# Performance work log

Hardware: AMD Instinct MI355X
Metric: run time of the kernel (lower is better)

Reference implementation:

```python
import jax, jax.numpy as jnp
import numpy as np
from jax import lax

EPS = 1e-3  # Keras BatchNormalization default epsilon
DN = ('NHWC', 'HWIO', 'NHWC')


def _bn(x, gamma, beta, mean, var):
    inv = gamma * lax.rsqrt(var + EPS)
    return x * inv + (beta - mean * inv)


def setup_inputs() -> dict:
    key = jax.random.key(0)
    ks = jax.random.split(key, 5)
    B, H, W, C = 32, 56, 56, 256
    G, CG = 32, 4  # cardinality, channels per group
    CM = G * CG    # 128 mid channels
    x = jax.random.normal(ks[0], (B, H, W, C), jnp.float32)
    # 32 branch 1x1 convs (256->4 each) stacked -> one 256->128 conv
    w1 = jax.random.normal(ks[1], (1, 1, C, CM), jnp.float32) * 0.05
    b1 = jnp.zeros((CM,), jnp.float32)
    g1 = jnp.ones((CM,), jnp.float32)
    be1 = jnp.zeros((CM,), jnp.float32)
    m1 = jnp.zeros((CM,), jnp.float32)
    v1 = jnp.ones((CM,), jnp.float32)
    # 32 branch 3x3 convs (4->4 each) stacked -> grouped conv kernel [3,3,4,128]
    w2 = jax.random.normal(ks[2], (3, 3, CG, CM), jnp.float32) * 0.1
    b2 = jnp.zeros((CM,), jnp.float32)
    g2 = jnp.ones((CM,), jnp.float32)
    be2 = jnp.zeros((CM,), jnp.float32)
    m2 = jnp.zeros((CM,), jnp.float32)
    v2 = jnp.ones((CM,), jnp.float32)
    # final 1x1 conv 128 -> 256
    w3 = jax.random.normal(ks[3], (1, 1, CM, C), jnp.float32) * 0.05
    b3 = jnp.zeros((C,), jnp.float32)
    return dict(x=x, w1=w1, b1=b1, g1=g1, be1=be1, m1=m1, v1=v1,
                w2=w2, b2=b2, g2=g2, be2=be2, m2=m2, v2=v2,
                w3=w3, b3=b3)


def reference(x, w1, b1, g1, be1, m1, v1, w2, b2, g2, be2, m2, v2, w3, b3):
    # branch 1x1 convs fused: conv 256 -> 128
    h = lax.conv_general_dilated(x, w1, (1, 1), 'SAME', dimension_numbers=DN) + b1
    h = jax.nn.relu(_bn(h, g1, be1, m1, v1))
    # branch 3x3 convs fused: grouped conv, 32 groups of 4 channels
    h = lax.conv_general_dilated(h, w2, (1, 1), 'SAME', dimension_numbers=DN,
                                 feature_group_count=32) + b2
    h = jax.nn.relu(_bn(h, g2, be2, m2, v2))
    # Dropout(0.2) is identity at inference
    # final 1x1 conv 128 -> 256, residual add, relu
    out = lax.conv_general_dilated(h, w3, (1, 1), 'SAME', dimension_numbers=DN) + b3
    return jax.nn.relu(out + x)
```

## Files before the change

### kernel.cpp

```cpp
#include <hip/hip_runtime.h>
#include <stdint.h>

typedef unsigned short u16;
typedef unsigned int   u32;
typedef __attribute__((ext_vector_type(8))) short bf16x8;
typedef __attribute__((ext_vector_type(4))) float f32x4;

#define EPS 1e-3f
#define NB 32
#define HW 56
#define CI 256
#define CM 128
#define PIX (NB*HW*HW)

__device__ __forceinline__ float asf(u32 i){ union{u32 u; float f;} t; t.u=i; return t.f; }
__device__ __forceinline__ u16 f2bf(float f){
  union{float f; u32 u;} t; t.f = f;
  u32 x = t.u;
  return (u16)((x + 0x7fffu + ((x>>16)&1u)) >> 16);
}

__global__ __launch_bounds__(256) void kprep(
    const float* __restrict__ w1, const float* __restrict__ b1, const float* __restrict__ g1,
    const float* __restrict__ be1, const float* __restrict__ m1, const float* __restrict__ v1,
    const float* __restrict__ b2, const float* __restrict__ g2,
    const float* __restrict__ be2, const float* __restrict__ m2, const float* __restrict__ v2,
    const float* __restrict__ w3,
    u16* __restrict__ w1s, u16* __restrict__ w3s,
    float* __restrict__ A1, float* __restrict__ B1,
    float* __restrict__ A2, float* __restrict__ B2){
  int i = blockIdx.x*256 + threadIdx.x;
  if (i < 32768){
    {
      int j = i & 7, lane = (i >> 3) & 63, kt = (i >> 9) & 7, t = i >> 12;
      int col = lane & 15, quad = lane >> 4;
      int n = t*16 + col, k = kt*32 + quad*8 + j;
      w1s[i] = f2bf(w1[k*CM + n]);
    }
    {
      int j = i & 7, lane = (i >> 3) & 63, kc = (i >> 9) & 3, t = i >> 11;
      int col = lane & 15, quad = lane >> 4;
      int n = t*16 + col, k = kc*32 + quad*8 + j;
      w3s[i] = f2bf(w3[k*CI + n]);
    }
  }
  if (i < 128){
    float s1 = g1[i] * rsqrtf(v1[i] + EPS);
    A1[i] = s1;
    B1[i] = b1[i]*s1 + be1[i] - m1[i]*s1;
    float s2 = g2[i] * rsqrtf(v2[i] + EPS);
    A2[i] = s2;
    B2[i] = b2[i]*s2 + be2[i] - m2[i]*s2;
  }
}

__global__ __launch_bounds__(256, 3) void k1(const float* __restrict__ x,
    const u16* __restrict__ w1s, const float* __restrict__ A1v,
    const float* __restrict__ B1v, u16* __restrict__ h1){
  __shared__ __align__(16) u16 outw[128*136];
  const int tid  = threadIdx.x;
  const int lane = tid & 63, wv = tid >> 6;
  const int col  = lane & 15, quad = lane >> 4;
  const long p0 = (long)blockIdx.x * 128;
  f32x4 acc[2][8];
  #pragma unroll
  for (int a = 0; a < 2; a++)
    #pragma unroll
    for (int b = 0; b < 8; b++){ acc[a][b][0]=0.f; acc[a][b][1]=0.f; acc[a][b][2]=0.f; acc[a][b][3]=0.f; }
  const float* xb = x + (p0 + wv*32 + col)*CI + quad*8;
  for (int kt = 0; kt < 8; kt++){
    bf16x8 bfr[8];
    #pragma unroll
    for (int nt = 0; nt < 8; nt++)
      bfr[nt] = *(const bf16x8*)(w1s + (size_t)((nt*8 + kt)*64 + lane)*8);
    #pragma unroll
    for (int mt = 0; mt < 2; mt++){
      const float* xp = xb + mt*16*CI + kt*32;
      float4 v0 = *(const float4*)xp;
      float4 v1 = *(const float4*)(xp + 4);
      union{ bf16x8 v; u32 w[4]; } af;
      af.w[0] = (u32)f2bf(v0.x) | ((u32)f2bf(v0.y) << 16);
      af.w[1] = (u32)f2bf(v0.z) | ((u32)f2bf(v0.w) << 16);
      af.w[2] = (u32)f2bf(v1.x) | ((u32)f2bf(v1.y) << 16);
      af.w[3] = (u32)f2bf(v1.z) | ((u32)f2bf(v1.w) << 16);
      #pragma unroll
      for (int nt = 0; nt < 8; nt++)
        acc[mt][nt] = __builtin_amdgcn_mfma_f32_16x16x32_bf16(af.v, bfr[nt], acc[mt][nt], 0, 0, 0);
    }
  }
  #pragma unroll
  for (int nt = 0; nt < 8; nt++){
    int n = nt*16 + col;
    float a1 = A1v[n], b1v = B1v[n];
    #pragma unroll
    for (int mt = 0; mt < 2; mt++)
      #pragma unroll
      for (int reg = 0; reg < 4; reg++){
        int m = wv*32 + mt*16 + quad*4 + reg;
        outw[m*136 + n] = f2bf(fmaxf(acc[mt][nt][reg]*a1 + b1v, 0.f));
      }
  }
  __syncthreads();
  #pragma unroll
  for (int r = 0; r < 8; r++){
    int idx = r*256 + tid;
    int m = idx >> 4, u4 = idx & 15;
    uint4 v = *(const uint4*)(outw + m*136 + u4*8);
    *(uint4*)(h1 + (p0+m)*CM + u4*8) = v;
  }
}

#define LSH1 132
#define LSH2 136
__global__ __launch_bounds__(512, 4) void k23(const u16* __restrict__ h1,
    const float* __restrict__ w2, const float* __restrict__ A2v,
    const float* __restrict__ B2v, const u16* __restrict__ w3s,
    const float* __restrict__ b3, const float* __restrict__ x,
    float* __restrict__ out){
  __shared__ __align__(16) char smem[3*HW*LSH1*2 + 4608*4];
  u16*  tile = (u16*)smem;
  u16*  h2t  = (u16*)smem;
  float* pre = (float*)smem;
  float* wsh = (float*)(smem + 3*HW*LSH1*2);

  const int tid = threadIdx.x;
  const int bid = blockIdx.x;
  const int blk = (bid & 7)*224 + (bid >> 3);
  const int y0 = blk % HW;
  const long p0 = (long)blk * HW;

  for (int i = tid; i < 1152; i += 512)
    ((float4*)wsh)[i] = ((const float4*)w2)[i];
  #pragma unroll
  for (int r = 0; r < 3; r++){
    const int yy = y0 + r - 1;
    const bool valid = (yy >= 0 && yy < HW);
    const uint4* src = (const uint4*)(h1 + (long)(blk - y0 + yy)*HW*CM);
    for (int i = tid; i < 896; i += 512){
      uint4 v = make_uint4(0u,0u,0u,0u);
      if (valid) v = src[i];
      int px = i >> 4, ch = (i & 15)*8;
      u16* d = tile + (r*HW + px)*LSH1 + ch;
      *(uint2*)d     = make_uint2(v.x, v.y);
      *(uint2*)(d+4) = make_uint2(v.z, v.w);
    }
  }
  __syncthreads();

  float4 xr[4];
  #pragma unroll
  for (int it = 0; it < 4; it++){
    int i = tid + it*512;
    if (i < 1792){
      int m = i >> 5, f4 = i & 31;
      xr[it] = *(const float4*)(x + (p0+m)*CI + f4*4);
    }
  }

  const int q = tid >> 6, pos = tid & 63;
  const bool act = pos < HW;
  u16 ov[16];
  if (act){
    int ixo[3]; u32 mk[3];
    #pragma unroll
    for (int kx = 0; kx < 3; kx++){
      int c = pos + kx - 1;
      ixo[kx] = (c < 0 ? 0 : (c > 55 ? 55 : c)) * LSH1;
      mk[kx] = (c >= 0 && c < HW) ? 0xffffffffu : 0u;
    }
    #pragma unroll
    for (int gi = 0; gi < 4; gi++){
      const int cb = q*16 + gi*4;
      float a0=0.f, a1=0.f, a2=0.f, a3=0.f;
      #pragma unroll
      for (int ky = 0; ky < 3; ky++){
        const u16* trow = tile + ky*HW*LSH1 + cb;
        #pragma unroll
        for (int kx = 0; kx < 3; kx++){
          uint2 hv = *(const uint2*)(trow + ixo[kx]);
          u32 hx = hv.x & mk[kx], hy = hv.y & mk[kx];
          float i0 = asf(hx<<16), i1 = asf(hx&0xffff0000u);
          float i2 = asf(hy<<16), i3 = asf(hy&0xffff0000u);
          const float* wp = wsh + ((ky*3+kx)*4)*CM + cb;
          float4 w0  = *(const float4*)(wp);
          float4 w1v = *(const float4*)(wp+CM);
          float4 w2v = *(const float4*)(wp+2*CM);
          float4 w3v = *(const float4*)(wp+3*CM);
          a0 += i0*w0.x + i1*w1v.x + i2*w2v.x + i3*w3v.x;
          a1 += i0*w0.y + i1*w1v.y + i2*w2v.y + i3*w3v.y;
          a2 += i0*w0.z + i1*w1v.z + i2*w2v.z + i3*w3v.z;
          a3 += i0*w0.w + i1*w1v.w + i2*w2v.w + i3*w3v.w;
        }
      }
      float av[4] = {a0, a1, a2, a3};
      #pragma unroll
      for (int co = 0; co < 4; co++){
        int c = cb + co;
        ov[gi*4+co] = f2bf(fmaxf(av[co]*A2v[c] + B2v[c], 0.f));
      }
    }
  }
  __syncthreads();

  if (act){
    uint4 pk0, pk1;
    pk0.x = (u32)ov[0]  | ((u32)ov[1]<<16);
    pk0.y = (u32)ov[2]  | ((u32)ov[3]<<16);
    pk0.z = (u32)ov[4]  | ((u32)ov[5]<<16);
    pk0.w = (u32)ov[6]  | ((u32)ov[7]<<16);
    pk1.x = (u32)ov[8]  | ((u32)ov[9]<<16);
    pk1.y = (u32)ov[10] | ((u32)ov[11]<<16);
    pk1.z = (u32)ov[12] | ((u32)ov[13]<<16);
    pk1.w = (u32)ov[14] | ((u32)ov[15]<<16);
    u16* op = h2t + pos*LSH2 + q*16;
    *(uint4*)op     = pk0;
    *(uint4*)(op+8) = pk1;
  }
  for (int i = tid; i < 544; i += 512)
    ((u32*)(h2t + 56*LSH2))[i] = 0u;
  __syncthreads();

  const int lane = tid & 63, wv = tid >> 6;
  const int col  = lane & 15, quad = lane >> 4;
  f32x4 acc3[4][2];
  #pragma unroll
  for (int a = 0; a < 4; a++)
    #pragma unroll
    for (int b = 0; b < 2; b++){ acc3[a][b][0]=0.f; acc3[a][b][1]=0.f; acc3[a][b][2]=0.f; acc3[a][b][3]=0.f; }
  float bias[2];
  #pragma unroll
  for (int nt = 0; nt < 2; nt++) bias[nt] = b3[wv*32 + nt*16 + col];
  #pragma unroll
  for (int kc = 0; kc < 4; kc++){
    bf16x8 bfr[2], af[4];
    #pragma unroll
    for (int nt = 0; nt < 2; nt++)
      bfr[nt] = *(const bf16x8*)(w3s + (size_t)(((wv*2+nt)*4 + kc)*64 + lane)*8);
    #pragma unroll
    for (int mt = 0; mt < 4; mt++)
      af[mt] = *(const bf16x8*)(h2t + (mt*16 + col)*LSH2 + kc*32 + quad*8);
    #pragma unroll
    for (int mt = 0; mt < 4; mt++)
      #pragma unroll
      for (int nt = 0; nt < 2; nt++)
        acc3[mt][nt] = __builtin_amdgcn_mfma_f32_16x16x32_bf16(af[mt], bfr[nt], acc3[mt][nt], 0, 0, 0);
  }
  __syncthreads();

  if (wv < 4){
    #pragma unroll
    for (int mt = 0; mt < 4; mt++)
      #pragma unroll
      for (int nt = 0; nt < 2; nt++)
        #pragma unroll
        for (int reg = 0; reg < 4; reg++){
          int m = mt*16 + quad*4 + reg;
          pre[m*132 + (wv&3)*32 + nt*16 + col] = acc3[mt][nt][reg] + bias[nt];
        }
  }
  __syncthreads();

  float4 xr2[4];
  #pragma unroll
  for (int it = 0; it < 4; it++){
    int i = tid + it*512;
    if (i < 1792){
      int m = i >> 5, f4 = i & 31;
      xr2[it] = *(const float4*)(x + (p0+m)*CI + 128 + f4*4);
    }
  }
  #pragma unroll
  for (int it = 0; it < 4; it++){
    int i = tid + it*512;
    if (i < 1792){
      int m = i >> 5, f4 = i & 31;
      float4 pv = *(const float4*)(pre + m*132 + f4*4);
      float4 o;
      o.x = fmaxf(pv.x + xr[it].x, 0.f);
      o.y = fmaxf(pv.y + xr[it].y, 0.f);
      o.z = fmaxf(pv.z + xr[it].z, 0.f);
      o.w = fmaxf(pv.w + xr[it].w, 0.f);
      *(float4*)(out + (p0+m)*CI + f4*4) = o;
    }
  }
  __syncthreads();

  if (wv >= 4){
    #pragma unroll
    for (int mt = 0; mt < 4; mt++)
      #pragma unroll
      for (int nt = 0; nt < 2; nt++)
        #pragma unroll
        for (int reg = 0; reg < 4; reg++){
          int m = mt*16 + quad*4 + reg;
          pre[m*132 + (wv&3)*32 + nt*16 + col] = acc3[mt][nt][reg] + bias[nt];
        }
  }
  __syncthreads();
  #pragma unroll
  for (int it = 0; it < 4; it++){
    int i = tid + it*512;
    if (i < 1792){
      int m = i >> 5, f4 = i & 31;
      float4 pv = *(const float4*)(pre + m*132 + f4*4);
      float4 o;
      o.x = fmaxf(pv.x + xr2[it].x, 0.f);
      o.y = fmaxf(pv.y + xr2[it].y, 0.f);
      o.z = fmaxf(pv.z + xr2[it].z, 0.f);
      o.w = fmaxf(pv.w + xr2[it].w, 0.f);
      *(float4*)(out + (p0+m)*CI + 128 + f4*4) = o;
    }
  }
}

extern "C" void kernel_launch(void* const* d_in, const int* in_sizes, int n_in,
                              void* d_out, int out_size, void* d_ws, size_t ws_size,
                              hipStream_t stream){
  (void)in_sizes; (void)n_in; (void)out_size; (void)ws_size;
  const float* x   = (const float*)d_in[0];
  const float* w1  = (const float*)d_in[1];
  const float* b1  = (const float*)d_in[2];
  const float* g1  = (const float*)d_in[3];
  const float* be1 = (const float*)d_in[4];
  const float* m1  = (const float*)d_in[5];
  const float* v1  = (const float*)d_in[6];
  const float* w2  = (const float*)d_in[7];
  const float* b2  = (const float*)d_in[8];
  const float* g2  = (const float*)d_in[9];
  const float* be2 = (const float*)d_in[10];
  const float* m2  = (const float*)d_in[11];
  const float* v2  = (const float*)d_in[12];
  const float* w3  = (const float*)d_in[13];
  const float* b3  = (const float*)d_in[14];

  char* ws = (char*)d_ws;
  u16* h1  = (u16*)ws;
  u16* w1s = (u16*)(ws + (size_t)PIX*CM*2);
  u16* w3s = w1s + 32768;
  float* A1 = (float*)(w3s + 32768);
  float* B1 = A1 + 128;
  float* A2 = B1 + 128;
  float* B2 = A2 + 128;

  kprep<<<128, 256, 0, stream>>>(w1,b1,g1,be1,m1,v1,b2,g2,be2,m2,v2,w3,
                                 w1s,w3s,A1,B1,A2,B2);
  k1<<<PIX/128, 256, 0, stream>>>(x, w1s, A1, B1, h1);
  k23<<<NB*HW, 512, 0, stream>>>(h1, w2, A2, B2, w3s, b3, x, (float*)d_out);
}
```

Measured before the change: 287.6 us.

## Stage x tile in swizzled LDS as bf16 in k1, widen to 512 threads

k1 now loads each 128-pixel block of x with coalesced float4 reads across the full row, converts it to bf16, and stores it into an XOR-swizzled LDS tile before the MFMA loop. The block grows to 8 waves, each computing a 32x64 output sub-tile. Before, each lane gathered strided 32-byte pieces of x directly from global memory. The aim is better global coalescing and more waves to hide latency, at the cost of a 64KB LDS footprint that limits occupancy. k23 drops its launch-bounds occupancy hint from 4 to 2 and loads the second-half residual x values at use time instead of prefetching them into registers, which lowers register pressure but exposes that load latency.

```diff
diff --git a/kernel.cpp b/kernel.cpp
--- a/kernel.cpp
+++ b/kernel.cpp
@@ -54,56 +54,73 @@
   }
 }
 
-__global__ __launch_bounds__(256, 3) void k1(const float* __restrict__ x,
+__global__ __launch_bounds__(512, 2) void k1(const float* __restrict__ x,
     const u16* __restrict__ w1s, const float* __restrict__ A1v,
     const float* __restrict__ B1v, u16* __restrict__ h1){
-  __shared__ __align__(16) u16 outw[128*136];
+  __shared__ __align__(16) char smem[65536];
+  u16* outw = (u16*)smem;
   const int tid  = threadIdx.x;
   const int lane = tid & 63, wv = tid >> 6;
   const int col  = lane & 15, quad = lane >> 4;
   const long p0 = (long)blockIdx.x * 128;
-  f32x4 acc[2][8];
+
+  {
+    const int c4 = lane;
+    const int swz = wv << 4;
+    const float* xp = x + (p0 + wv)*CI + c4*4;
+    char* dp = smem + (size_t)wv*512 + ((c4*8) ^ swz);
+    #pragma unroll
+    for (int i = 0; i < 16; i++){
+      float4 v = *(const float4*)(xp + (size_t)i*8*CI);
+      u32 lo = (u32)f2bf(v.x) | ((u32)f2bf(v.y) << 16);
+      u32 hi = (u32)f2bf(v.z) | ((u32)f2bf(v.w) << 16);
+      *(uint2*)(dp + (size_t)i*8*512) = make_uint2(lo, hi);
+    }
+  }
+  f32x4 acc[2][4];
   #pragma unroll
   for (int a = 0; a < 2; a++)
     #pragma unroll
-    for (int b = 0; b < 8; b++){ acc[a][b][0]=0.f; acc[a][b][1]=0.f; acc[a][b][2]=0.f; acc[a][b][3]=0.f; }
-  const float* xb = x + (p0 + wv*32 + col)*CI + quad*8;
+    for (int b = 0; b < 4; b++){ acc[a][b][0]=0.f; acc[a][b][1]=0.f; acc[a][b][2]=0.f; acc[a][b][3]=0.f; }
+  __syncthreads();
+
+  const int mg = wv >> 1, nh = wv & 1;
+  #pragma unroll
   for (int kt = 0; kt < 8; kt++){
-    bf16x8 bfr[8];
-    #pragma unroll
-    for (int nt = 0; nt < 8; nt++)
-      bfr[nt] = *(const bf16x8*)(w1s + (size_t)((nt*8 + kt)*64 + lane)*8);
+    bf16x8 bfr[4], af[2];
+    #pragma unroll
+    for (int nt = 0; nt < 4; nt++)
+      bfr[nt] = *(const bf16x8*)(w1s + (size_t)(((nh*4+nt)*8 + kt)*64 + lane)*8);
     #pragma unroll
     for (int mt = 0; mt < 2; mt++){
-      const float* xp = xb + mt*16*CI + kt*32;
-      float4 v0 = *(const float4*)xp;
-      float4 v1 = *(const float4*)(xp + 4);
-      union{ bf16x8 v; u32 w[4]; } af;
-      af.w[0] = (u32)f2bf(v0.x) | ((u32)f2bf(v0.y) << 16);
-      af.w[1] = (u32)f2bf(v0.z) | ((u32)f2bf(v0.w) << 16);
-      af.w[2] = (u32)f2bf(v1.x) | ((u32)f2bf(v1.y) << 16);
-      af.w[3] = (u32)f2bf(v1.z) | ((u32)f2bf(v1.w) << 16);
-      #pragma unroll
-      for (int nt = 0; nt < 8; nt++)
-        acc[mt][nt] = __builtin_amdgcn_mfma_f32_16x16x32_bf16(af.v, bfr[nt], acc[mt][nt], 0, 0, 0);
-    }
-  }
-  #pragma unroll
-  for (int nt = 0; nt < 8; nt++){
-    int n = nt*16 + col;
+      int row = mg*32 + mt*16 + col;
+      int byte = row*512 + ((kt*64 + quad*16) ^ ((row & 7) << 4));
+      af[mt] = *(const bf16x8*)(smem + byte);
+    }
+    #pragma unroll
+    for (int mt = 0; mt < 2; mt++)
+      #pragma unroll
+      for (int nt = 0; nt < 4; nt++)
+        acc[mt][nt] = __builtin_amdgcn_mfma_f32_16x16x32_bf16(af[mt], bfr[nt], acc[mt][nt], 0, 0, 0);
+  }
+  __syncthreads();
+
+  #pragma unroll
+  for (int nt = 0; nt < 4; nt++){
+    int n = nh*64 + nt*16 + col;
     float a1 = A1v[n], b1v = B1v[n];
     #pragma unroll
     for (int mt = 0; mt < 2; mt++)
       #pragma unroll
       for (int reg = 0; reg < 4; reg++){
-        int m = wv*32 + mt*16 + quad*4 + reg;
+        int m = mg*32 + mt*16 + quad*4 + reg;
         outw[m*136 + n] = f2bf(fmaxf(acc[mt][nt][reg]*a1 + b1v, 0.f));
       }
   }
   __syncthreads();
   #pragma unroll
-  for (int r = 0; r < 8; r++){
-    int idx = r*256 + tid;
+  for (int r = 0; r < 4; r++){
+    int idx = r*512 + tid;
     int m = idx >> 4, u4 = idx & 15;
     uint4 v = *(const uint4*)(outw + m*136 + u4*8);
     *(uint4*)(h1 + (p0+m)*CM + u4*8) = v;
@@ -112,7 +129,7 @@
 
 #define LSH1 132
 #define LSH2 136
-__global__ __launch_bounds__(512, 4) void k23(const u16* __restrict__ h1,
+__global__ __launch_bounds__(512, 2) void k23(const u16* __restrict__ h1,
     const float* __restrict__ w2, const float* __restrict__ A2v,
     const float* __restrict__ B2v, const u16* __restrict__ w3s,
     const float* __restrict__ b3, const float* __restrict__ x,
@@ -259,16 +276,6 @@
         }
   }
   __syncthreads();
-
-  float4 xr2[4];
-  #pragma unroll
-  for (int it = 0; it < 4; it++){
-    int i = tid + it*512;
-    if (i < 1792){
-      int m = i >> 5, f4 = i & 31;
-      xr2[it] = *(const float4*)(x + (p0+m)*CI + 128 + f4*4);
-    }
-  }
   #pragma unroll
   for (int it = 0; it < 4; it++){
     int i = tid + it*512;
@@ -302,12 +309,13 @@
     int i = tid + it*512;
     if (i < 1792){
       int m = i >> 5, f4 = i & 31;
+      float4 xv = *(const float4*)(x + (p0+m)*CI + 128 + f4*4);
       float4 pv = *(const float4*)(pre + m*132 + f4*4);
       float4 o;
-      o.x = fmaxf(pv.x + xr2[it].x, 0.f);
-      o.y = fmaxf(pv.y + xr2[it].y, 0.f);
-      o.z = fmaxf(pv.z + xr2[it].z, 0.f);
-      o.w = fmaxf(pv.w + xr2[it].w, 0.f);
+      o.x = fmaxf(pv.x + xv.x, 0.f);
+      o.y = fmaxf(pv.y + xv.y, 0.f);
+      o.z = fmaxf(pv.z + xv.z, 0.f);
+      o.w = fmaxf(pv.w + xv.w, 0.f);
       *(float4*)(out + (p0+m)*CI + 128 + f4*4) = o;
     }
   }
@@ -344,6 +352,6 @@
 
   kprep<<<128, 256, 0, stream>>>(w1,b1,g1,be1,m1,v1,b2,g2,be2,m2,v2,w3,
                                  w1s,w3s,A1,B1,A2,B2);
-  k1<<<PIX/128, 256, 0, stream>>>(x, w1s, A1, B1, h1);
+  k1<<<PIX/128, 512, 0, stream>>>(x, w1s, A1, B1, h1);
   k23<<<NB*HW, 512, 0, stream>>>(h1, w2, A2, B2, w3s, b3, x, (float*)d_out);
 }
```

After: 284.1 us. About the same (-1.2%).
